# Performance work log

Measured on AMD Instinct MI355X. Metric: run time of the kernel, lower is better.

Reference implementation:

```python
import jax, jax.numpy as jnp
import numpy as np

DIM = 768
NUM_HEADS = 12
HEAD_DIM = DIM // NUM_HEADS
SCALE = HEAD_DIM ** -0.5


def setup_inputs() -> dict:
    key = jax.random.key(0)
    k1, k2, k3, k4, k5 = jax.random.split(key, 5)
    B, N = 8, 2048
    x = jax.random.normal(k1, (B, N, DIM), dtype=jnp.float32)
    mask = jax.random.randint(k2, (B, N), 0, 2, dtype=jnp.int32)
    # ensure at least one valid key per batch row to avoid all -inf softmax rows
    mask = mask.at[:, 0].set(1)
    w_qkv = jax.random.normal(k3, (DIM, 3 * DIM), dtype=jnp.float32) * (DIM ** -0.5)
    w_proj = jax.random.normal(k4, (DIM, DIM), dtype=jnp.float32) * (DIM ** -0.5)
    b_proj = jax.random.normal(k5, (DIM,), dtype=jnp.float32) * 0.02
    return {"x": x, "mask": mask, "w_qkv": w_qkv, "w_proj": w_proj, "b_proj": b_proj}


def reference(x, mask, w_qkv, w_proj, b_proj):
    B, N, C = x.shape
    qkv = (x @ w_qkv).reshape(B, N, 3, NUM_HEADS, HEAD_DIM)
    qkv = jnp.transpose(qkv, (2, 0, 3, 1, 4))  # [3, B, H, N, D]
    q, k, v = qkv[0], qkv[1], qkv[2]
    q = q * SCALE
    # fp32 upcast for scores (inputs already fp32; explicit for fidelity)
    attn = jnp.einsum('bhqd,bhkd->bhqk', q.astype(jnp.float32), k.astype(jnp.float32))
    key_mask = mask.astype(bool)[:, None, None, :]  # [B,1,1,N]
    attn = jnp.where(key_mask, attn, -jnp.inf)
    attn = jax.nn.softmax(attn, axis=-1).astype(x.dtype)
    out = jnp.einsum('bhqk,bhkd->bhqd', attn, v)  # [B,H,N,D]
    out = jnp.transpose(out, (0, 2, 1, 3)).reshape(B, N, C)
    return out @ w_proj + b_proj
```

## Files before the change

kernel.cpp:

```cpp
#include <hip/hip_runtime.h>
#include <hip/hip_bf16.h>
#include <stdint.h>

#define NHEAD 12
#define SEQ   2048
#define NB    8
#define MTOK  (NB*SEQ)
#define DIMC  768
#define QKVN  (3*DIMC)

typedef __attribute__((ext_vector_type(8))) short bf16x8;
typedef __attribute__((ext_vector_type(4))) float f32x4;
typedef __attribute__((ext_vector_type(16))) float f32x16;
typedef __attribute__((ext_vector_type(4))) unsigned short u16x4;
typedef __attribute__((ext_vector_type(4))) unsigned int u32x4;

typedef const __attribute__((address_space(1))) char glb_char;
typedef __attribute__((address_space(3))) char lds_char;

__device__ __forceinline__ unsigned short f2bf(float f) {
  union { float f; unsigned u; } v; v.f = f;
  return (unsigned short)((v.u + 0x7FFFu + ((v.u >> 16) & 1u)) >> 16);
}

__device__ __forceinline__ void gload_lds16(const void* g, void* l) {
  __builtin_amdgcn_global_load_lds((glb_char*)g, (lds_char*)l, 16, 0, 0);
}

__device__ __forceinline__ unsigned cvtpk_bf16(float lo, float hi) {
  unsigned d;
  asm("v_cvt_pk_bf16_f32 %0, %1, %2" : "=v"(d) : "v"(lo), "v"(hi));
  return d;
}

#define QSCALE 0.18033688011112042f
#define MASKBIAS -30000.0f

__global__ void __launch_bounds__(256, 8)
cvt_bf16_kernel(const float* __restrict__ in,
                unsigned short* __restrict__ out, int n4) {
  int idx = blockIdx.x * blockDim.x + threadIdx.x;
  int stride = gridDim.x * blockDim.x;
  for (int i = idx; i < n4; i += stride) {
    float4 v = ((const float4*)in)[i];
    u16x4 o;
    o.x = f2bf(v.x); o.y = f2bf(v.y); o.z = f2bf(v.z); o.w = f2bf(v.w);
    ((u16x4*)out)[i] = o;
  }
}

__global__ void __launch_bounds__(256, 4)
maskscan_kernel(const int* __restrict__ mask, int* __restrict__ posmap,
                float* __restrict__ mbias_c, int* __restrict__ nvalid) {
  __shared__ int sums[256];
  __shared__ int btot;
  const int b = blockIdx.x, t = threadIdx.x;
  const int* m = mask + b * SEQ;
  int loc[8];
  int s = 0;
  #pragma unroll
  for (int i = 0; i < 8; i++) { loc[i] = (m[t * 8 + i] != 0) ? 1 : 0; s += loc[i]; }
  sums[t] = s;
  __syncthreads();
  for (int off = 1; off < 256; off <<= 1) {
    int v = (t >= off) ? sums[t - off] : 0;
    __syncthreads();
    sums[t] += v;
    __syncthreads();
  }
  int excl = sums[t] - s;
  if (t == 255) btot = sums[255];
  __syncthreads();
  const int nv = btot;
  #pragma unroll
  for (int i = 0; i < 8; i++) {
    posmap[b * SEQ + t * 8 + i] = loc[i] ? excl : -1;
    excl += loc[i];
  }
  for (int j = t; j < SEQ; j += 256)
    mbias_c[b * SEQ + j] = (j < nv) ? 0.0f : MASKBIAS;
  if (t == 0) nvalid[b] = nv;
}

__global__ void __launch_bounds__(256, 8)
zerotail_kernel(unsigned short* __restrict__ kc, unsigned short* __restrict__ vc,
                const int* __restrict__ nvalid) {
  const int bh = blockIdx.x, t = threadIdx.x;
  const int b = bh / NHEAD;
  const int nv = nvalid[b];
  const int pad = (nv + 63) & ~63;
  const int nz = pad - nv;
  if (nz == 0) return;
  unsigned short* kcb = kc + (size_t)bh * SEQ * 64;
  unsigned short* vcb = vc + (size_t)bh * 64 * SEQ;
  for (int i = t; i < nz * 64; i += 256) {
    int r = i >> 6, d = i & 63;
    kcb[(nv + r) * 64 + d] = 0;
  }
  for (int i = t; i < 64 * nz; i += 256) {
    int d = i / nz, c = i - d * nz;
    vcb[(size_t)d * SEQ + nv + c] = 0;
  }
}

__global__ void __launch_bounds__(256, 8)
transpose_cvt_kernel(const float* __restrict__ in,
                     unsigned short* __restrict__ out,
                     int R, int C) {
  __shared__ float tile[32][33];
  int c0 = blockIdx.x * 32, r0 = blockIdx.y * 32;
  int tx = threadIdx.x & 31, ty = threadIdx.x >> 5;
  #pragma unroll
  for (int i = 0; i < 32; i += 8)
    tile[ty + i][tx] = in[(size_t)(r0 + ty + i) * C + c0 + tx];
  __syncthreads();
  #pragma unroll
  for (int i = 0; i < 32; i += 8)
    out[(size_t)(c0 + ty + i) * R + r0 + tx] = f2bf(tile[tx][ty + i]);
}

__global__ void __launch_bounds__(256, 3)
qkv_gemm_kernel(const unsigned short* __restrict__ xb,
                const unsigned short* __restrict__ wT,
                unsigned short* __restrict__ qo,
                unsigned short* __restrict__ ko,
                unsigned short* __restrict__ vto,
                const int* __restrict__ posmap) {
  __shared__ short lA[3][128 * 32];
  __shared__ short lB[3][128 * 32];
  const int t = threadIdx.x;
  const int lane = t & 63, w = t >> 6;
  const int m0 = blockIdx.x * 128;
  const int n0 = blockIdx.y * 128;
  const int wr = (w >> 1) * 64, wc = (w & 1) * 64;
  const int l15 = lane & 15, lg = lane >> 4;
  const int sr = t >> 2;
  const int sc = t & 3;

  auto STAGE = [&](int k0, int bsel) {
    #pragma unroll
    for (int i = 0; i < 2; i++) {
      int row = i * 64 + sr;
      int cb = (sc ^ ((row >> 1) & 3)) * 8;
      gload_lds16(xb + (size_t)(m0 + row) * DIMC + k0 + cb,
                  (char*)lA + bsel * 8192 + i * 4096 + w * 1024);
      gload_lds16(wT + (size_t)(n0 + row) * DIMC + k0 + cb,
                  (char*)lB + bsel * 8192 + i * 4096 + w * 1024);
    }
  };

  f32x4 acc[4][4] = {};
  const int NT = DIMC / 32;

  STAGE(0, 0);
  STAGE(32, 1);

  int cur = 0;
  for (int kt = 0; kt < NT; ++kt) {
    if (kt < NT - 1) asm volatile("s_waitcnt vmcnt(4)" ::: "memory");
    else             asm volatile("s_waitcnt vmcnt(0)" ::: "memory");
    __builtin_amdgcn_s_barrier();
    if (kt + 2 < NT) {
      int nb = cur + 2; if (nb >= 3) nb -= 3;
      STAGE((kt + 2) * 32, nb);
    }
    const short* A = &lA[cur][0];
    const short* B = &lB[cur][0];

    bf16x8 af[4], bfr[4];
    #pragma unroll
    for (int mi = 0; mi < 4; mi++) {
      int m = wr + mi * 16 + l15;
      af[mi] = *(const bf16x8*)&A[m * 32 + ((lg ^ ((m >> 1) & 3)) << 3)];
    }
    #pragma unroll
    for (int nj = 0; nj < 4; nj++) {
      int n = wc + nj * 16 + l15;
      bfr[nj] = *(const bf16x8*)&B[n * 32 + ((lg ^ ((n >> 1) & 3)) << 3)];
    }
    __builtin_amdgcn_s_setprio(1);
    #pragma unroll
    for (int mi = 0; mi < 4; mi++)
      #pragma unroll
      for (int nj = 0; nj < 4; nj++)
        acc[mi][nj] = __builtin_amdgcn_mfma_f32_16x16x32_bf16(af[mi], bfr[nj], acc[mi][nj], 0, 0, 0);
    __builtin_amdgcn_s_setprio(0);

    cur = (cur == 2) ? 0 : cur + 1;
  }

  #pragma unroll
  for (int mi = 0; mi < 4; mi++) {
    int tok0 = m0 + wr + mi * 16 + 4 * lg;
    int bb = tok0 >> 11;
    int nn0 = tok0 & 2047;
    int pm[4];
    #pragma unroll
    for (int r = 0; r < 4; r++) pm[r] = posmap[tok0 + r];
    #pragma unroll
    for (int nj = 0; nj < 4; nj++) {
      int col = n0 + wc + nj * 16 + l15;
      int which = col / DIMC;
      int ch = col - which * DIMC;
      int hh = ch >> 6, dd = ch & 63;
      size_t hb = (size_t)(bb * NHEAD + hh);
      if (which == 0) {
        size_t base = (hb * SEQ + nn0) * 64 + dd;
        #pragma unroll
        for (int r = 0; r < 4; r++)
          qo[base + (size_t)r * 64] = f2bf(acc[mi][nj][r] * QSCALE);
      } else if (which == 1) {
        #pragma unroll
        for (int r = 0; r < 4; r++)
          if (pm[r] >= 0)
            ko[(hb * SEQ + pm[r]) * 64 + dd] = f2bf(acc[mi][nj][r]);
      } else {
        #pragma unroll
        for (int r = 0; r < 4; r++)
          if (pm[r] >= 0)
            vto[(hb * 64 + dd) * SEQ + pm[r]] = f2bf(acc[mi][nj][r]);
      }
    }
  }
}

__global__ void __launch_bounds__(256, 4)
attn_kernel(const unsigned short* __restrict__ qbuf,
            const unsigned short* __restrict__ kbuf,
            const unsigned short* __restrict__ vtbuf,
            const float* __restrict__ mbias_c,
            const int* __restrict__ nvalid,
            unsigned short* __restrict__ ao) {
  __shared__ short lKV[2][8192];
  __shared__ float lmask[2][64];
  const int t = threadIdx.x, lane = t & 63, w = t >> 6;
  const int l31 = lane & 31, hi = lane >> 5;
  const int bid = blockIdx.x;
  const int qt = bid / 96;
  const int bh = bid - qt * 96;
  const int b = bh / NHEAD, h = bh - b * NHEAD;
  const int q0 = qt * 128 + w * 32;
  const unsigned short* qb = qbuf + (size_t)bh * SEQ * 64;
  const unsigned short* kb = kbuf + (size_t)bh * SEQ * 64;
  const unsigned short* vb = vtbuf + (size_t)bh * 64 * SEQ;
  const float* mb = mbias_c + b * SEQ;
  const int ntiles = (nvalid[b] + 63) >> 6;

  auto STAGE = [&](int tile, int bsel) {
    int kv0 = tile * 64;
    #pragma unroll
    for (int i = 0; i < 2; i++) {
      int c = i * 4 + w;
      gload_lds16(kb + (size_t)(kv0 + lane) * 64 + c * 8,
                  (char*)lKV + bsel * 16384 + c * 1024);
      gload_lds16(vb + (size_t)lane * SEQ + kv0 + c * 8,
                  (char*)lKV + bsel * 16384 + 8192 + c * 1024);
    }
    if (w == 0)
      __builtin_amdgcn_global_load_lds((glb_char*)(mb + tile * 64 + lane),
                                       (lds_char*)&lmask[bsel][0], 4, 0, 0);
  };

  bf16x8 qf[4];
  #pragma unroll
  for (int dblk = 0; dblk < 4; dblk++)
    qf[dblk] = *(const bf16x8*)(qb + (size_t)(q0 + l31) * 64 + dblk * 16 + hi * 8);

  f32x16 O[2] = {};
  float ls[4] = {0.f, 0.f, 0.f, 0.f};

  STAGE(0, 0);
  __syncthreads();

  for (int it = 0; it < ntiles; ++it) {
    const int bsel = it & 1;
    const short* Kb = &lKV[bsel][0];
    const short* Vb = &lKV[bsel][4096];
    if (it + 1 < ntiles) STAGE(it + 1, bsel ^ 1);

    #pragma unroll
    for (int kb2 = 0; kb2 < 2; kb2++) {
      f32x4 mb4[4];
      #pragma unroll
      for (int g = 0; g < 4; g++)
        mb4[g] = *(const f32x4*)&lmask[bsel][kb2 * 32 + g * 8 + hi * 4];
      f32x16 S;
      #pragma unroll
      for (int r = 0; r < 16; r++) S[r] = mb4[r >> 2][r & 3];

      __builtin_amdgcn_s_setprio(1);
      #pragma unroll
      for (int dblk = 0; dblk < 4; dblk++) {
        bf16x8 kf = *(const bf16x8*)&Kb[(dblk * 2 + hi) * 512 + (kb2 * 32 + l31) * 8];
        S = __builtin_amdgcn_mfma_f32_32x32x16_bf16(kf, qf[dblk], S, 0, 0, 0);
      }
      __builtin_amdgcn_s_setprio(0);

      float p[16];
      #pragma unroll
      for (int r = 0; r < 16; r++) p[r] = __builtin_amdgcn_exp2f(S[r]);
      #pragma unroll
      for (int r = 0; r < 16; r++) ls[r & 3] += p[r];

      #pragma unroll
      for (int half = 0; half < 2; half++) {
        unsigned a0 = cvtpk_bf16(p[half * 8 + 0], p[half * 8 + 1]);
        unsigned a1 = cvtpk_bf16(p[half * 8 + 2], p[half * 8 + 3]);
        unsigned a2 = cvtpk_bf16(p[half * 8 + 4], p[half * 8 + 5]);
        unsigned a3 = cvtpk_bf16(p[half * 8 + 6], p[half * 8 + 7]);
        asm("v_permlane32_swap_b32 %0, %1" : "+v"(a0), "+v"(a2));
        asm("v_permlane32_swap_b32 %0, %1" : "+v"(a1), "+v"(a3));
        union { u32x4 u; bf16x8 f; } cv;
        cv.u = (u32x4){a0, a1, a2, a3};
        __builtin_amdgcn_s_setprio(1);
        #pragma unroll
        for (int dt = 0; dt < 2; dt++) {
          bf16x8 vf = *(const bf16x8*)&Vb[(kb2 * 4 + half * 2 + hi) * 512 + (dt * 32 + l31) * 8];
          O[dt] = __builtin_amdgcn_mfma_f32_32x32x16_bf16(cv.f, vf, O[dt], 0, 0, 0);
        }
        __builtin_amdgcn_s_setprio(0);
      }
    }

    if (it + 1 < ntiles) {
      asm volatile("s_waitcnt vmcnt(0)" ::: "memory");
      __builtin_amdgcn_s_barrier();
    }
  }

  float* lrs = (float*)&lKV[0][0];
  float tot = (ls[0] + ls[1]) + (ls[2] + ls[3]);
  tot += __shfl_xor(tot, 32);
  lrs[w * 32 + l31] = tot;

  float inv[16];
  #pragma unroll
  for (int r = 0; r < 16; r++)
    inv[r] = 1.0f / lrs[w * 32 + (r & 3) + 8 * (r >> 2) + 4 * hi];

  #pragma unroll
  for (int dt = 0; dt < 2; dt++) {
    #pragma unroll
    for (int r = 0; r < 16; r++) {
      int qrow = q0 + (r & 3) + 8 * (r >> 2) + 4 * hi;
      size_t base = ((size_t)(b * SEQ + qrow)) * DIMC + h * 64 + dt * 32 + l31;
      ao[base] = __bfloat16_as_ushort(__float2bfloat16(O[dt][r] * inv[r]));
    }
  }
}

__global__ void __launch_bounds__(256, 3)
proj_gemm_kernel(const unsigned short* __restrict__ ab,
                 const unsigned short* __restrict__ wT,
                 const float* __restrict__ bias,
                 float* __restrict__ out) {
  __shared__ short lA[3][128 * 32];
  __shared__ short lB[3][128 * 32];
  const int t = threadIdx.x;
  const int lane = t & 63, w = t >> 6;
  const int m0 = blockIdx.x * 128;
  const int n0 = blockIdx.y * 128;
  const int wr = (w >> 1) * 64, wc = (w & 1) * 64;
  const int l15 = lane & 15, lg = lane >> 4;
  const int sr = t >> 2;
  const int sc = t & 3;

  auto STAGE = [&](int k0, int bsel) {
    #pragma unroll
    for (int i = 0; i < 2; i++) {
      int row = i * 64 + sr;
      int cb = (sc ^ ((row >> 1) & 3)) * 8;
      gload_lds16(ab + (size_t)(m0 + row) * DIMC + k0 + cb,
                  (char*)lA + bsel * 8192 + i * 4096 + w * 1024);
      gload_lds16(wT + (size_t)(n0 + row) * DIMC + k0 + cb,
                  (char*)lB + bsel * 8192 + i * 4096 + w * 1024);
    }
  };

  f32x4 acc[4][4] = {};
  const int NT = DIMC / 32;

  STAGE(0, 0);
  STAGE(32, 1);

  int cur = 0;
  for (int kt = 0; kt < NT; ++kt) {
    if (kt < NT - 1) asm volatile("s_waitcnt vmcnt(4)" ::: "memory");
    else             asm volatile("s_waitcnt vmcnt(0)" ::: "memory");
    __builtin_amdgcn_s_barrier();
    if (kt + 2 < NT) {
      int nb = cur + 2; if (nb >= 3) nb -= 3;
      STAGE((kt + 2) * 32, nb);
    }
    const short* A = &lA[cur][0];
    const short* B = &lB[cur][0];

    bf16x8 af[4], bfr[4];
    #pragma unroll
    for (int mi = 0; mi < 4; mi++) {
      int m = wr + mi * 16 + l15;
      af[mi] = *(const bf16x8*)&A[m * 32 + ((lg ^ ((m >> 1) & 3)) << 3)];
    }
    #pragma unroll
    for (int nj = 0; nj < 4; nj++) {
      int n = wc + nj * 16 + l15;
      bfr[nj] = *(const bf16x8*)&B[n * 32 + ((lg ^ ((n >> 1) & 3)) << 3)];
    }
    __builtin_amdgcn_s_setprio(1);
    #pragma unroll
    for (int mi = 0; mi < 4; mi++)
      #pragma unroll
      for (int nj = 0; nj < 4; nj++)
        acc[mi][nj] = __builtin_amdgcn_mfma_f32_16x16x32_bf16(af[mi], bfr[nj], acc[mi][nj], 0, 0, 0);
    __builtin_amdgcn_s_setprio(0);

    cur = (cur == 2) ? 0 : cur + 1;
  }

  #pragma unroll
  for (int mi = 0; mi < 4; mi++) {
    int row0 = m0 + wr + mi * 16 + 4 * lg;
    #pragma unroll
    for (int nj = 0; nj < 4; nj++) {
      int col = n0 + wc + nj * 16 + l15;
      float bv = bias[col];
      #pragma unroll
      for (int r = 0; r < 4; r++)
        out[(size_t)(row0 + r) * DIMC + col] = acc[mi][nj][r] + bv;
    }
  }
}

extern "C" void kernel_launch(void* const* d_in, const int* in_sizes, int n_in,
                              void* d_out, int out_size, void* d_ws, size_t ws_size,
                              hipStream_t stream) {
  const float* x      = (const float*)d_in[0];
  const int*   mask   = (const int*)d_in[1];
  const float* w_qkv  = (const float*)d_in[2];
  const float* w_proj = (const float*)d_in[3];
  const float* b_proj = (const float*)d_in[4];
  float* out = (float*)d_out;

  unsigned short* ws = (unsigned short*)d_ws;
  unsigned short* xb     = ws;
  unsigned short* wqkvT  = xb    + (size_t)MTOK * DIMC;
  unsigned short* wprojT = wqkvT + (size_t)QKVN * DIMC;
  unsigned short* qbuf   = wprojT + (size_t)DIMC * DIMC;
  unsigned short* kbuf   = qbuf  + (size_t)MTOK * DIMC;
  unsigned short* vtbuf  = kbuf  + (size_t)MTOK * DIMC;
  float*          mbias_c = (float*)(vtbuf + (size_t)MTOK * DIMC);
  int*            posmap  = (int*)(mbias_c + MTOK);
  int*            nvalid  = posmap + MTOK;
  unsigned short* aob    = xb;

  cvt_bf16_kernel<<<2048, 256, 0, stream>>>(x, xb, MTOK * DIMC / 4);
  maskscan_kernel<<<NB, 256, 0, stream>>>(mask, posmap, mbias_c, nvalid);
  transpose_cvt_kernel<<<dim3(QKVN / 32, DIMC / 32), 256, 0, stream>>>(w_qkv, wqkvT, DIMC, QKVN);
  transpose_cvt_kernel<<<dim3(DIMC / 32, DIMC / 32), 256, 0, stream>>>(w_proj, wprojT, DIMC, DIMC);
  qkv_gemm_kernel<<<dim3(128, 18), 256, 0, stream>>>(xb, wqkvT, qbuf, kbuf, vtbuf, posmap);
  zerotail_kernel<<<NB * NHEAD, 256, 0, stream>>>(kbuf, vtbuf, nvalid);
  attn_kernel<<<1536, 256, 0, stream>>>(qbuf, kbuf, vtbuf, mbias_c, nvalid, aob);
  proj_gemm_kernel<<<dim3(128, 6), 256, 0, stream>>>(aob, wprojT, b_proj, out);
}
```

Before: 215.0 us.

## Process two 32-row query tiles per wave in attention to reuse K/V fragments

Each wave now handles 64 query rows (two 32-row MFMA tiles) instead of 32, so each block covers 256 queries and the grid is halved to 768 blocks. Every K and V fragment read from LDS feeds two MFMAs, which halves LDS traffic and global K/V staging per query. The cost is higher register pressure (launch bounds lowered to 3 waves/SIMD) and fewer blocks, which may reduce occupancy and latency hiding on a machine with many CUs. A __syncthreads is added before reusing the K/V LDS buffer for the row sums.

After: 310.6 us. 44.4% more time.

```diff
diff --git a/kernel.cpp b/kernel.cpp
--- a/kernel.cpp
+++ b/kernel.cpp
@@ -224,7 +224,7 @@
   }
 }
 
-__global__ void __launch_bounds__(256, 4)
+__global__ void __launch_bounds__(256, 3)
 attn_kernel(const unsigned short* __restrict__ qbuf,
             const unsigned short* __restrict__ kbuf,
             const unsigned short* __restrict__ vtbuf,
@@ -239,7 +239,7 @@
   const int qt = bid / 96;
   const int bh = bid - qt * 96;
   const int b = bh / NHEAD, h = bh - b * NHEAD;
-  const int q0 = qt * 128 + w * 32;
+  const int q0 = qt * 256 + w * 64;
   const unsigned short* qb = qbuf + (size_t)bh * SEQ * 64;
   const unsigned short* kb = kbuf + (size_t)bh * SEQ * 64;
   const unsigned short* vb = vtbuf + (size_t)bh * 64 * SEQ;
@@ -261,13 +261,16 @@
                                        (lds_char*)&lmask[bsel][0], 4, 0, 0);
   };
 
-  bf16x8 qf[4];
-  #pragma unroll
-  for (int dblk = 0; dblk < 4; dblk++)
-    qf[dblk] = *(const bf16x8*)(qb + (size_t)(q0 + l31) * 64 + dblk * 16 + hi * 8);
-
-  f32x16 O[2] = {};
-  float ls[4] = {0.f, 0.f, 0.f, 0.f};
+  bf16x8 qf[2][4];
+  #pragma unroll
+  for (int mi = 0; mi < 2; mi++)
+    #pragma unroll
+    for (int dblk = 0; dblk < 4; dblk++)
+      qf[mi][dblk] = *(const bf16x8*)(qb + (size_t)(q0 + mi * 32 + l31) * 64 + dblk * 16 + hi * 8);
+
+  f32x16 O[2][2] = {};
+  float lsA[4] = {0.f, 0.f, 0.f, 0.f};
+  float lsB[4] = {0.f, 0.f, 0.f, 0.f};
 
   STAGE(0, 0);
   __syncthreads();
@@ -284,42 +287,70 @@
       #pragma unroll
       for (int g = 0; g < 4; g++)
         mb4[g] = *(const f32x4*)&lmask[bsel][kb2 * 32 + g * 8 + hi * 4];
-      f32x16 S;
-      #pragma unroll
-      for (int r = 0; r < 16; r++) S[r] = mb4[r >> 2][r & 3];
+      f32x16 S0, S1;
+      #pragma unroll
+      for (int r = 0; r < 16; r++) { float bv = mb4[r >> 2][r & 3]; S0[r] = bv; S1[r] = bv; }
 
       __builtin_amdgcn_s_setprio(1);
       #pragma unroll
       for (int dblk = 0; dblk < 4; dblk++) {
         bf16x8 kf = *(const bf16x8*)&Kb[(dblk * 2 + hi) * 512 + (kb2 * 32 + l31) * 8];
-        S = __builtin_amdgcn_mfma_f32_32x32x16_bf16(kf, qf[dblk], S, 0, 0, 0);
+        S0 = __builtin_amdgcn_mfma_f32_32x32x16_bf16(kf, qf[0][dblk], S0, 0, 0, 0);
+        S1 = __builtin_amdgcn_mfma_f32_32x32x16_bf16(kf, qf[1][dblk], S1, 0, 0, 0);
       }
       __builtin_amdgcn_s_setprio(0);
 
-      float p[16];
-      #pragma unroll
-      for (int r = 0; r < 16; r++) p[r] = __builtin_amdgcn_exp2f(S[r]);
-      #pragma unroll
-      for (int r = 0; r < 16; r++) ls[r & 3] += p[r];
-
+      bf16x8 pfr[2][2];
+      {
+        float p[16];
+        #pragma unroll
+        for (int r = 0; r < 16; r++) p[r] = __builtin_amdgcn_exp2f(S0[r]);
+        #pragma unroll
+        for (int r = 0; r < 16; r++) lsA[r & 3] += p[r];
+        #pragma unroll
+        for (int half = 0; half < 2; half++) {
+          unsigned a0 = cvtpk_bf16(p[half * 8 + 0], p[half * 8 + 1]);
+          unsigned a1 = cvtpk_bf16(p[half * 8 + 2], p[half * 8 + 3]);
+          unsigned a2 = cvtpk_bf16(p[half * 8 + 4], p[half * 8 + 5]);
+          unsigned a3 = cvtpk_bf16(p[half * 8 + 6], p[half * 8 + 7]);
+          asm("v_permlane32_swap_b32 %0, %1" : "+v"(a0), "+v"(a2));
+          asm("v_permlane32_swap_b32 %0, %1" : "+v"(a1), "+v"(a3));
+          union { u32x4 u; bf16x8 f; } cv;
+          cv.u = (u32x4){a0, a1, a2, a3};
+          pfr[0][half] = cv.f;
+        }
+      }
+      {
+        float p[16];
+        #pragma unroll
+        for (int r = 0; r < 16; r++) p[r] = __builtin_amdgcn_exp2f(S1[r]);
+        #pragma unroll
+        for (int r = 0; r < 16; r++) lsB[r & 3] += p[r];
+        #pragma unroll
+        for (int half = 0; half < 2; half++) {
+          unsigned a0 = cvtpk_bf16(p[half * 8 + 0], p[half * 8 + 1]);
+          unsigned a1 = cvtpk_bf16(p[half * 8 + 2], p[half * 8 + 3]);
+          unsigned a2 = cvtpk_bf16(p[half * 8 + 4], p[half * 8 + 5]);
+          unsigned a3 = cvtpk_bf16(p[half * 8 + 6], p[half * 8 + 7]);
+          asm("v_permlane32_swap_b32 %0, %1" : "+v"(a0), "+v"(a2));
+          asm("v_permlane32_swap_b32 %0, %1" : "+v"(a1), "+v"(a3));
+          union { u32x4 u; bf16x8 f; } cv;
+          cv.u = (u32x4){a0, a1, a2, a3};
+          pfr[1][half] = cv.f;
+        }
+      }
+
+      __builtin_amdgcn_s_setprio(1);
       #pragma unroll
       for (int half = 0; half < 2; half++) {
-        unsigned a0 = cvtpk_bf16(p[half * 8 + 0], p[half * 8 + 1]);
-        unsigned a1 = cvtpk_bf16(p[half * 8 + 2], p[half * 8 + 3]);
-        unsigned a2 = cvtpk_bf16(p[half * 8 + 4], p[half * 8 + 5]);
-        unsigned a3 = cvtpk_bf16(p[half * 8 + 6], p[half * 8 + 7]);
-        asm("v_permlane32_swap_b32 %0, %1" : "+v"(a0), "+v"(a2));
-        asm("v_permlane32_swap_b32 %0, %1" : "+v"(a1), "+v"(a3));
-        union { u32x4 u; bf16x8 f; } cv;
-        cv.u = (u32x4){a0, a1, a2, a3};
-        __builtin_amdgcn_s_setprio(1);
         #pragma unroll
         for (int dt = 0; dt < 2; dt++) {
           bf16x8 vf = *(const bf16x8*)&Vb[(kb2 * 4 + half * 2 + hi) * 512 + (dt * 32 + l31) * 8];
-          O[dt] = __builtin_amdgcn_mfma_f32_32x32x16_bf16(cv.f, vf, O[dt], 0, 0, 0);
+          O[0][dt] = __builtin_amdgcn_mfma_f32_32x32x16_bf16(pfr[0][half], vf, O[0][dt], 0, 0, 0);
+          O[1][dt] = __builtin_amdgcn_mfma_f32_32x32x16_bf16(pfr[1][half], vf, O[1][dt], 0, 0, 0);
         }
-        __builtin_amdgcn_s_setprio(0);
-      }
+      }
+      __builtin_amdgcn_s_setprio(0);
     }
 
     if (it + 1 < ntiles) {
@@ -328,23 +359,27 @@
     }
   }
 
+  __syncthreads();
   float* lrs = (float*)&lKV[0][0];
-  float tot = (ls[0] + ls[1]) + (ls[2] + ls[3]);
-  tot += __shfl_xor(tot, 32);
-  lrs[w * 32 + l31] = tot;
-
-  float inv[16];
-  #pragma unroll
-  for (int r = 0; r < 16; r++)
-    inv[r] = 1.0f / lrs[w * 32 + (r & 3) + 8 * (r >> 2) + 4 * hi];
-
-  #pragma unroll
-  for (int dt = 0; dt < 2; dt++) {
-    #pragma unroll
-    for (int r = 0; r < 16; r++) {
-      int qrow = q0 + (r & 3) + 8 * (r >> 2) + 4 * hi;
-      size_t base = ((size_t)(b * SEQ + qrow)) * DIMC + h * 64 + dt * 32 + l31;
-      ao[base] = __bfloat16_as_ushort(__float2bfloat16(O[dt][r] * inv[r]));
+  float t0 = (lsA[0] + lsA[1]) + (lsA[2] + lsA[3]);
+  t0 += __shfl_xor(t0, 32);
+  float t1 = (lsB[0] + lsB[1]) + (lsB[2] + lsB[3]);
+  t1 += __shfl_xor(t1, 32);
+  lrs[w * 64 + l31] = t0;
+  lrs[w * 64 + 32 + l31] = t1;
+
+  #pragma unroll
+  for (int mi = 0; mi < 2; mi++) {
+    #pragma unroll
+    for (int dt = 0; dt < 2; dt++) {
+      #pragma unroll
+      for (int r = 0; r < 16; r++) {
+        int idx = (r & 3) + 8 * (r >> 2) + 4 * hi;
+        float inv = 1.0f / lrs[w * 64 + mi * 32 + idx];
+        int qrow = q0 + mi * 32 + idx;
+        size_t base = ((size_t)(b * SEQ + qrow)) * DIMC + h * 64 + dt * 32 + l31;
+        ao[base] = __bfloat16_as_ushort(__float2bfloat16(O[mi][dt][r] * inv));
+      }
     }
   }
 }
@@ -459,6 +494,6 @@
   transpose_cvt_kernel<<<dim3(DIMC / 32, DIMC / 32), 256, 0, stream>>>(w_proj, wprojT, DIMC, DIMC);
   qkv_gemm_kernel<<<dim3(128, 18), 256, 0, stream>>>(xb, wqkvT, qbuf, kbuf, vtbuf, posmap);
   zerotail_kernel<<<NB * NHEAD, 256, 0, stream>>>(kbuf, vtbuf, nvalid);
-  attn_kernel<<<1536, 256, 0, stream>>>(qbuf, kbuf, vtbuf, mbias_c, nvalid, aob);
+  attn_kernel<<<768, 256, 0, stream>>>(qbuf, kbuf, vtbuf, mbias_c, nvalid, aob);
   proj_gemm_kernel<<<dim3(128, 6), 256, 0, stream>>>(aob, wprojT, b_proj, out);
 }
```

## Split QKV GEMM and compute K/V only for unmasked tokens via gathered rows

Applied to the files above, without the earlier changes.

The fused QKV projection is split into a Q GEMM over all tokens and a K/V GEMM that gathers only the valid (unmasked) token rows through a source-index map built in the mask scan. Tiles beyond the valid count return early, so about half of the K/V projection work is skipped for a random mask. V stores become packed 4-wide writes because positions are now contiguous. This adds a second GEMM launch and gathered A-tile loads, and also inserts a barrier before LDS reuse in the attention epilogue.

Measured after the change: 201.9 us. 6.1% less time.

```diff
diff --git a/kernel.cpp b/kernel.cpp
--- a/kernel.cpp
+++ b/kernel.cpp
@@ -51,7 +51,8 @@
 
 __global__ void __launch_bounds__(256, 4)
 maskscan_kernel(const int* __restrict__ mask, int* __restrict__ posmap,
-                float* __restrict__ mbias_c, int* __restrict__ nvalid) {
+                int* __restrict__ srcidx, float* __restrict__ mbias_c,
+                int* __restrict__ nvalid) {
   __shared__ int sums[256];
   __shared__ int btot;
   const int b = blockIdx.x, t = threadIdx.x;
@@ -75,10 +76,13 @@
   #pragma unroll
   for (int i = 0; i < 8; i++) {
     posmap[b * SEQ + t * 8 + i] = loc[i] ? excl : -1;
+    if (loc[i]) srcidx[b * SEQ + excl] = t * 8 + i;
     excl += loc[i];
   }
-  for (int j = t; j < SEQ; j += 256)
+  for (int j = t; j < SEQ; j += 256) {
     mbias_c[b * SEQ + j] = (j < nv) ? 0.0f : MASKBIAS;
+    if (j >= nv) srcidx[b * SEQ + j] = 0;
+  }
   if (t == 0) nvalid[b] = nv;
 }
 
@@ -120,12 +124,9 @@
 }
 
 __global__ void __launch_bounds__(256, 3)
-qkv_gemm_kernel(const unsigned short* __restrict__ xb,
-                const unsigned short* __restrict__ wT,
-                unsigned short* __restrict__ qo,
-                unsigned short* __restrict__ ko,
-                unsigned short* __restrict__ vto,
-                const int* __restrict__ posmap) {
+q_gemm_kernel(const unsigned short* __restrict__ xb,
+              const unsigned short* __restrict__ wT,
+              unsigned short* __restrict__ qo) {
   __shared__ short lA[3][128 * 32];
   __shared__ short lB[3][128 * 32];
   const int t = threadIdx.x;
@@ -194,32 +195,121 @@
     int tok0 = m0 + wr + mi * 16 + 4 * lg;
     int bb = tok0 >> 11;
     int nn0 = tok0 & 2047;
-    int pm[4];
-    #pragma unroll
-    for (int r = 0; r < 4; r++) pm[r] = posmap[tok0 + r];
     #pragma unroll
     for (int nj = 0; nj < 4; nj++) {
       int col = n0 + wc + nj * 16 + l15;
-      int which = col / DIMC;
-      int ch = col - which * DIMC;
+      int hh = col >> 6, dd = col & 63;
+      size_t base = (((size_t)(bb * NHEAD + hh)) * SEQ + nn0) * 64 + dd;
+      #pragma unroll
+      for (int r = 0; r < 4; r++)
+        qo[base + (size_t)r * 64] = f2bf(acc[mi][nj][r] * QSCALE);
+    }
+  }
+}
+
+__global__ void __launch_bounds__(256, 3)
+kv_gemm_kernel(const unsigned short* __restrict__ xb,
+               const unsigned short* __restrict__ wT,
+               unsigned short* __restrict__ ko,
+               unsigned short* __restrict__ vto,
+               const int* __restrict__ srcidx,
+               const int* __restrict__ nvalid) {
+  const int b = blockIdx.z;
+  const int m0 = blockIdx.x * 128;
+  if (m0 >= ((nvalid[b] + 127) & ~127)) return;
+  __shared__ short lA[3][128 * 32];
+  __shared__ short lB[3][128 * 32];
+  const int t = threadIdx.x;
+  const int lane = t & 63, w = t >> 6;
+  const int n0 = blockIdx.y * 128;
+  const int wr = (w >> 1) * 64, wc = (w & 1) * 64;
+  const int l15 = lane & 15, lg = lane >> 4;
+  const int sr = t >> 2;
+  const int sc = t & 3;
+
+  const int srow0 = srcidx[b * SEQ + m0 + sr];
+  const int srow1 = srcidx[b * SEQ + m0 + 64 + sr];
+  const unsigned short* xbb = xb + (size_t)b * SEQ * DIMC;
+  const unsigned short* wTkv = wT + (size_t)DIMC * DIMC;
+
+  auto STAGE = [&](int k0, int bsel) {
+    int cb = (sc ^ ((sr >> 1) & 3)) * 8;
+    gload_lds16(xbb + (size_t)srow0 * DIMC + k0 + cb,
+                (char*)lA + bsel * 8192 + w * 1024);
+    gload_lds16(xbb + (size_t)srow1 * DIMC + k0 + cb,
+                (char*)lA + bsel * 8192 + 4096 + w * 1024);
+    #pragma unroll
+    for (int i = 0; i < 2; i++) {
+      int row = i * 64 + sr;
+      int cb2 = (sc ^ ((row >> 1) & 3)) * 8;
+      gload_lds16(wTkv + (size_t)(n0 + row) * DIMC + k0 + cb2,
+                  (char*)lB + bsel * 8192 + i * 4096 + w * 1024);
+    }
+  };
+
+  f32x4 acc[4][4] = {};
+  const int NT = DIMC / 32;
+
+  STAGE(0, 0);
+  STAGE(32, 1);
+
+  int cur = 0;
+  for (int kt = 0; kt < NT; ++kt) {
+    if (kt < NT - 1) asm volatile("s_waitcnt vmcnt(4)" ::: "memory");
+    else             asm volatile("s_waitcnt vmcnt(0)" ::: "memory");
+    __builtin_amdgcn_s_barrier();
+    if (kt + 2 < NT) {
+      int nb = cur + 2; if (nb >= 3) nb -= 3;
+      STAGE((kt + 2) * 32, nb);
+    }
+    const short* A = &lA[cur][0];
+    const short* B = &lB[cur][0];
+
+    bf16x8 af[4], bfr[4];
+    #pragma unroll
+    for (int mi = 0; mi < 4; mi++) {
+      int m = wr + mi * 16 + l15;
+      af[mi] = *(const bf16x8*)&A[m * 32 + ((lg ^ ((m >> 1) & 3)) << 3)];
+    }
+    #pragma unroll
+    for (int nj = 0; nj < 4; nj++) {
+      int n = wc + nj * 16 + l15;
+      bfr[nj] = *(const bf16x8*)&B[n * 32 + ((lg ^ ((n >> 1) & 3)) << 3)];
+    }
+    __builtin_amdgcn_s_setprio(1);
+    #pragma unroll
+    for (int mi = 0; mi < 4; mi++)
+      #pragma unroll
+      for (int nj = 0; nj < 4; nj++)
+        acc[mi][nj] = __builtin_amdgcn_mfma_f32_16x16x32_bf16(af[mi], bfr[nj], acc[mi][nj], 0, 0, 0);
+    __builtin_amdgcn_s_setprio(0);
+
+    cur = (cur == 2) ? 0 : cur + 1;
+  }
+
+  #pragma unroll
+  for (int mi = 0; mi < 4; mi++) {
+    int pos0 = m0 + wr + mi * 16 + 4 * lg;
+    #pragma unroll
+    for (int nj = 0; nj < 4; nj++) {
+      int col = n0 + wc + nj * 16 + l15;
+      int which = col >> 9;
+      int ch = (col >= DIMC) ? col - DIMC : col;
       int hh = ch >> 6, dd = ch & 63;
-      size_t hb = (size_t)(bb * NHEAD + hh);
-      if (which == 0) {
-        size_t base = (hb * SEQ + nn0) * 64 + dd;
+      size_t hb = (size_t)(b * NHEAD + hh);
+      if (col < DIMC) {
+        size_t base = (hb * SEQ + pos0) * 64 + dd;
         #pragma unroll
         for (int r = 0; r < 4; r++)
-          qo[base + (size_t)r * 64] = f2bf(acc[mi][nj][r] * QSCALE);
-      } else if (which == 1) {
-        #pragma unroll
-        for (int r = 0; r < 4; r++)
-          if (pm[r] >= 0)
-            ko[(hb * SEQ + pm[r]) * 64 + dd] = f2bf(acc[mi][nj][r]);
+          ko[base + (size_t)r * 64] = f2bf(acc[mi][nj][r]);
       } else {
-        #pragma unroll
-        for (int r = 0; r < 4; r++)
-          if (pm[r] >= 0)
-            vto[(hb * 64 + dd) * SEQ + pm[r]] = f2bf(acc[mi][nj][r]);
+        size_t base = (hb * 64 + dd) * SEQ + pos0;
+        u16x4 pk;
+        pk.x = f2bf(acc[mi][nj][0]); pk.y = f2bf(acc[mi][nj][1]);
+        pk.z = f2bf(acc[mi][nj][2]); pk.w = f2bf(acc[mi][nj][3]);
+        *(u16x4*)(vto + base) = pk;
       }
+      (void)which;
     }
   }
 }
@@ -328,6 +418,7 @@
     }
   }
 
+  __syncthreads();
   float* lrs = (float*)&lKV[0][0];
   float tot = (ls[0] + ls[1]) + (ls[2] + ls[3]);
   tot += __shfl_xor(tot, 32);
@@ -451,13 +542,15 @@
   float*          mbias_c = (float*)(vtbuf + (size_t)MTOK * DIMC);
   int*            posmap  = (int*)(mbias_c + MTOK);
   int*            nvalid  = posmap + MTOK;
+  int*            srcidx  = nvalid + 8;
   unsigned short* aob    = xb;
 
   cvt_bf16_kernel<<<2048, 256, 0, stream>>>(x, xb, MTOK * DIMC / 4);
-  maskscan_kernel<<<NB, 256, 0, stream>>>(mask, posmap, mbias_c, nvalid);
+  maskscan_kernel<<<NB, 256, 0, stream>>>(mask, posmap, srcidx, mbias_c, nvalid);
   transpose_cvt_kernel<<<dim3(QKVN / 32, DIMC / 32), 256, 0, stream>>>(w_qkv, wqkvT, DIMC, QKVN);
   transpose_cvt_kernel<<<dim3(DIMC / 32, DIMC / 32), 256, 0, stream>>>(w_proj, wprojT, DIMC, DIMC);
-  qkv_gemm_kernel<<<dim3(128, 18), 256, 0, stream>>>(xb, wqkvT, qbuf, kbuf, vtbuf, posmap);
+  q_gemm_kernel<<<dim3(128, 6), 256, 0, stream>>>(xb, wqkvT, qbuf);
+  kv_gemm_kernel<<<dim3(16, 12, NB), 256, 0, stream>>>(xb, wqkvT, kbuf, vtbuf, srcidx, nvalid);
   zerotail_kernel<<<NB * NHEAD, 256, 0, stream>>>(kbuf, vtbuf, nvalid);
   attn_kernel<<<1536, 256, 0, stream>>>(qbuf, kbuf, vtbuf, mbias_c, nvalid, aob);
   proj_gemm_kernel<<<dim3(128, 6), 256, 0, stream>>>(aob, wprojT, b_proj, out);
```
